# Kernel tuning notes

Hardware: AMD Instinct MI355X
Metric: run time of the kernel (lower is better)

The kernel has to match this reference:

```python
import jax, jax.numpy as jnp
import numpy as np

SIGMA_BOOST = 2.0   # sparse-hyper util.SIGMA_BOOST
EPSILON = 1e-6      # sparse-hyper util.EPSILON (10e-7)
B, N = 512, 16384   # batch, size


def setup_inputs() -> dict:
    key = jax.random.key(0)
    k1, k2, k3, k4, k5 = jax.random.split(key, 5)
    return {
        "x": jax.random.normal(k1, (B, N), jnp.float32),
        "noise": jax.random.normal(k2, (B, N, 2), jnp.float32),
        "pmeans": jax.random.normal(k3, (N, 2), jnp.float32),
        "psigmas": jax.random.normal(k4, (N,), jnp.float32),
        "pvalues": jax.random.normal(k5, (N,), jnp.float32),
    }


def reference(x, noise, pmeans, psigmas, pvalues):
    b, n = x.shape
    s = jnp.float32(n)  # square size (n, n); both dims equal
    # hyper(): transform_means = sigmoid * (size-1); transform_sigmas = (softplus(.+boost)+eps) * size
    means = jax.nn.sigmoid(pmeans)[None] * (s - 1.0)                    # (1, n, 2) -> bcast (b, n, 2)
    sigmas = (jax.nn.softplus(psigmas + SIGMA_BOOST) + EPSILON)[None, :, None] * s  # (1, n, 1)
    # Normal(means, sigmas).sample() -- non-differentiable sample
    samples = jax.lax.stop_gradient(means + sigmas * noise)             # (b, n, 2)
    # round, clamp to [0, n-1]
    indices = jnp.clip(jnp.round(samples).astype(jnp.int32), 0, n - 1)  # (b, n, 2)
    rows, cols = indices[..., 0], indices[..., 1]                       # (b, n) each
    values = jnp.broadcast_to(pvalues[None, :], (b, n))
    # sparse.contract: y[b, rows[b,t]] += values[b,t] * x[b, cols[b,t]]
    contrib = values * jnp.take_along_axis(x, cols, axis=1)             # (b, n)
    y = jnp.zeros((b, n), x.dtype).at[jnp.arange(b)[:, None], rows].add(contrib)
    return y
```

## Files before the change

### kernel.cpp

```cpp
#include <hip/hip_runtime.h>
#include <math.h>

#define SIGMA_BOOST 2.0f
#define EPSILON 1e-6f

typedef float vfloat4 __attribute__((ext_vector_type(4)));

__global__ void params_kernel(const float2* __restrict__ pmeans,
                              const float* __restrict__ psigmas,
                              const float* __restrict__ pvalues,
                              float4* __restrict__ params, int N) {
    int t = blockIdx.x * blockDim.x + threadIdx.x;
    if (t >= N) return;
    float2 pm = pmeans[t];
    float scale = (float)(N - 1);
    float m0 = __fmul_rn(__fdiv_rn(1.0f, __fadd_rn(1.0f, expf(-pm.x))), scale);
    float m1 = __fmul_rn(__fdiv_rn(1.0f, __fadd_rn(1.0f, expf(-pm.y))), scale);
    float z  = __fadd_rn(psigmas[t], SIGMA_BOOST);
    float sp = __fadd_rn(fmaxf(z, 0.0f), log1pf(expf(-fabsf(z))));
    float sg = __fmul_rn(__fadd_rn(sp, EPSILON), (float)N);
    params[t] = make_float4(m0, m1, sg, pvalues[t]);
}

__device__ __forceinline__ void sample_m(
        const float4 p, const float n0, const float n1,
        const float* __restrict__ xb, float* __restrict__ ly,
        const int iN1, const float fN1, float& acc0, float& accE) {
    float s0 = __fadd_rn(p.x, __fmul_rn(p.z, n0));
    float s1 = __fadd_rn(p.y, __fmul_rn(p.z, n1));
    int row = (int)fminf(fmaxf(rintf(s0), 0.0f), fN1);
    int col = (int)fminf(fmaxf(rintf(s1), 0.0f), fN1);
    float xv = xb[col];
    float ctr = __fmul_rn(p.w, xv);
    bool lo = (row == 0);
    bool hi = (row == iN1);
    if (!(lo | hi)) atomicAdd(&ly[row], ctr);
    acc0 = __fadd_rn(acc0, lo ? ctr : 0.0f);
    accE = __fadd_rn(accE, hi ? ctr : 0.0f);
}

template <bool INLINE_PARAMS>
__launch_bounds__(1024, 8)
__global__ void contract_kernel(const float* __restrict__ x,
                                const float2* __restrict__ noise,
                                const float4* __restrict__ params,
                                const float2* __restrict__ pmeans,
                                const float* __restrict__ psigmas,
                                const float* __restrict__ pvalues,
                                float* __restrict__ y, int N) {
    extern __shared__ float ly[];
    const int b = blockIdx.x;
    const int tid = threadIdx.x;
    const int nthr = blockDim.x;

    float4* ly4 = (float4*)ly;
    const int n4 = N >> 2;
    for (int i = tid; i < n4; i += nthr) ly4[i] = make_float4(0.f, 0.f, 0.f, 0.f);
    __syncthreads();

    const float* xb = x + (size_t)b * N;
    const float fN1 = (float)(N - 1);
    const int iN1 = N - 1;
    float acc0 = 0.0f, accE = 0.0f;

    if (!INLINE_PARAMS && ((N >> 1) % (2 * nthr)) == 0) {
        const vfloat4* nb4 = (const vfloat4*)(noise + (size_t)b * N);
        const int npairs = N >> 1;
        const int steps = npairs / (2 * nthr);
        int q0 = tid, q1 = tid + nthr;
        vfloat4 nzA = __builtin_nontemporal_load(&nb4[q0]);
        vfloat4 nzB = __builtin_nontemporal_load(&nb4[q1]);
        float4 pa = params[2 * q0];
        float4 pb = params[2 * q0 + 1];
        float4 pc = params[2 * q1];
        float4 pd = params[2 * q1 + 1];
        for (int s = 0; s < steps; ++s) {
            const vfloat4 cA = nzA, cB = nzB;
            const float4 qa = pa, qb = pb, qc = pc, qd = pd;
            q0 += 2 * nthr; q1 += 2 * nthr;
            if (s + 1 < steps) {
                nzA = __builtin_nontemporal_load(&nb4[q0]);
                nzB = __builtin_nontemporal_load(&nb4[q1]);
                pa = params[2 * q0];
                pb = params[2 * q0 + 1];
                pc = params[2 * q1];
                pd = params[2 * q1 + 1];
            }
            sample_m(qa, cA.x, cA.y, xb, ly, iN1, fN1, acc0, accE);
            sample_m(qb, cA.z, cA.w, xb, ly, iN1, fN1, acc0, accE);
            sample_m(qc, cB.x, cB.y, xb, ly, iN1, fN1, acc0, accE);
            sample_m(qd, cB.z, cB.w, xb, ly, iN1, fN1, acc0, accE);
        }
    } else {
        const float2* nb = noise + (size_t)b * N;
        for (int t = tid; t < N; t += nthr) {
            float4 p;
            if (INLINE_PARAMS) {
                float2 pm = pmeans[t];
                float scale = (float)(N - 1);
                p.x = __fmul_rn(__fdiv_rn(1.0f, __fadd_rn(1.0f, expf(-pm.x))), scale);
                p.y = __fmul_rn(__fdiv_rn(1.0f, __fadd_rn(1.0f, expf(-pm.y))), scale);
                float z  = __fadd_rn(psigmas[t], SIGMA_BOOST);
                float sp = __fadd_rn(fmaxf(z, 0.0f), log1pf(expf(-fabsf(z))));
                p.z = __fmul_rn(__fadd_rn(sp, EPSILON), (float)N);
                p.w = pvalues[t];
            } else {
                p = params[t];
            }
            float2 nz = nb[t];
            sample_m(p, nz.x, nz.y, xb, ly, iN1, fN1, acc0, accE);
        }
    }

    for (int off = 32; off > 0; off >>= 1) {
        acc0 = __fadd_rn(acc0, __shfl_down(acc0, off, 64));
        accE = __fadd_rn(accE, __shfl_down(accE, off, 64));
    }
    if ((tid & 63) == 0) {
        atomicAdd(&ly[0], acc0);
        atomicAdd(&ly[iN1], accE);
    }
    __syncthreads();

    const vfloat4* lv4 = (const vfloat4*)ly;
    vfloat4* yb4 = (vfloat4*)(y + (size_t)b * N);
    for (int i = tid; i < n4; i += nthr)
        __builtin_nontemporal_store(lv4[i], &yb4[i]);
}

extern "C" void kernel_launch(void* const* d_in, const int* in_sizes, int n_in,
                              void* d_out, int out_size, void* d_ws, size_t ws_size,
                              hipStream_t stream) {
    const float*  x       = (const float*)d_in[0];
    const float2* noise   = (const float2*)d_in[1];
    const float2* pmeans  = (const float2*)d_in[2];
    const float*  psigmas = (const float*)d_in[3];
    const float*  pvalues = (const float*)d_in[4];
    float* y = (float*)d_out;

    const int N = in_sizes[3];
    const int B = in_sizes[0] / N;

    const size_t params_bytes = (size_t)N * sizeof(float4);
    const bool use_ws = (ws_size >= params_bytes) && (d_ws != nullptr);

    const int block = 1024;
    const size_t lds_bytes = (size_t)N * sizeof(float);

    if (use_ws) {
        float4* params = (float4*)d_ws;
        params_kernel<<<(N + 255) / 256, 256, 0, stream>>>(pmeans, psigmas,
                                                           pvalues, params, N);
        contract_kernel<false><<<B, block, lds_bytes, stream>>>(
            x, noise, params, nullptr, nullptr, nullptr, y, N);
    } else {
        contract_kernel<true><<<B, block, lds_bytes, stream>>>(
            x, noise, nullptr, pmeans, psigmas, pvalues, y, N);
    }
}
```

Baseline: 150.1 us.

## Stage x in LDS for gathers and scatter atomics directly to global y

Swaps the roles of shared memory and global memory. Each block's row of x is now copied into LDS so the random column gathers read from LDS, while y is zeroed in global memory and the scatter-adds go straight to global y as atomics. This removes the LDS zero-fill and the final LDS-to-global copy of y. In exchange, every non-boundary contribution becomes a global atomic instead of an LDS atomic, which can cost much more per operation.

```diff
diff --git a/kernel.cpp b/kernel.cpp
--- a/kernel.cpp
+++ b/kernel.cpp
@@ -22,19 +22,19 @@
     params[t] = make_float4(m0, m1, sg, pvalues[t]);
 }
 
-__device__ __forceinline__ void sample_m(
+__device__ __forceinline__ void sample_g(
         const float4 p, const float n0, const float n1,
-        const float* __restrict__ xb, float* __restrict__ ly,
+        const float* __restrict__ lx, float* __restrict__ yb,
         const int iN1, const float fN1, float& acc0, float& accE) {
     float s0 = __fadd_rn(p.x, __fmul_rn(p.z, n0));
     float s1 = __fadd_rn(p.y, __fmul_rn(p.z, n1));
     int row = (int)fminf(fmaxf(rintf(s0), 0.0f), fN1);
     int col = (int)fminf(fmaxf(rintf(s1), 0.0f), fN1);
-    float xv = xb[col];
+    float xv = lx[col];
     float ctr = __fmul_rn(p.w, xv);
     bool lo = (row == 0);
     bool hi = (row == iN1);
-    if (!(lo | hi)) atomicAdd(&ly[row], ctr);
+    if (!(lo | hi)) atomicAdd(&yb[row], ctr);
     acc0 = __fadd_rn(acc0, lo ? ctr : 0.0f);
     accE = __fadd_rn(accE, hi ? ctr : 0.0f);
 }
@@ -48,17 +48,32 @@
                                 const float* __restrict__ psigmas,
                                 const float* __restrict__ pvalues,
                                 float* __restrict__ y, int N) {
-    extern __shared__ float ly[];
+    extern __shared__ float lx[];
     const int b = blockIdx.x;
     const int tid = threadIdx.x;
     const int nthr = blockDim.x;
 
-    float4* ly4 = (float4*)ly;
-    const int n4 = N >> 2;
-    for (int i = tid; i < n4; i += nthr) ly4[i] = make_float4(0.f, 0.f, 0.f, 0.f);
+    const float* xb = x + (size_t)b * N;
+    float* yb = y + (size_t)b * N;
+
+    if ((N & 3) == 0) {
+        const int n4 = N >> 2;
+        vfloat4* lx4 = (vfloat4*)lx;
+        const vfloat4* xb4 = (const vfloat4*)xb;
+        vfloat4* yb4 = (vfloat4*)yb;
+        const vfloat4 vz = {0.f, 0.f, 0.f, 0.f};
+        for (int i = tid; i < n4; i += nthr) {
+            lx4[i] = xb4[i];
+            yb4[i] = vz;
+        }
+    } else {
+        for (int i = tid; i < N; i += nthr) {
+            lx[i] = xb[i];
+            yb[i] = 0.0f;
+        }
+    }
     __syncthreads();
 
-    const float* xb = x + (size_t)b * N;
     const float fN1 = (float)(N - 1);
     const int iN1 = N - 1;
     float acc0 = 0.0f, accE = 0.0f;
@@ -86,10 +101,10 @@
                 pc = params[2 * q1];
                 pd = params[2 * q1 + 1];
             }
-            sample_m(qa, cA.x, cA.y, xb, ly, iN1, fN1, acc0, accE);
-            sample_m(qb, cA.z, cA.w, xb, ly, iN1, fN1, acc0, accE);
-            sample_m(qc, cB.x, cB.y, xb, ly, iN1, fN1, acc0, accE);
-            sample_m(qd, cB.z, cB.w, xb, ly, iN1, fN1, acc0, accE);
+            sample_g(qa, cA.x, cA.y, lx, yb, iN1, fN1, acc0, accE);
+            sample_g(qb, cA.z, cA.w, lx, yb, iN1, fN1, acc0, accE);
+            sample_g(qc, cB.x, cB.y, lx, yb, iN1, fN1, acc0, accE);
+            sample_g(qd, cB.z, cB.w, lx, yb, iN1, fN1, acc0, accE);
         }
     } else {
         const float2* nb = noise + (size_t)b * N;
@@ -108,7 +123,7 @@
                 p = params[t];
             }
             float2 nz = nb[t];
-            sample_m(p, nz.x, nz.y, xb, ly, iN1, fN1, acc0, accE);
+            sample_g(p, nz.x, nz.y, lx, yb, iN1, fN1, acc0, accE);
         }
     }
 
@@ -117,15 +132,9 @@
         accE = __fadd_rn(accE, __shfl_down(accE, off, 64));
     }
     if ((tid & 63) == 0) {
-        atomicAdd(&ly[0], acc0);
-        atomicAdd(&ly[iN1], accE);
+        atomicAdd(&yb[0], acc0);
+        atomicAdd(&yb[iN1], accE);
     }
-    __syncthreads();
-
-    const vfloat4* lv4 = (const vfloat4*)ly;
-    vfloat4* yb4 = (vfloat4*)(y + (size_t)b * N);
-    for (int i = tid; i < n4; i += nthr)
-        __builtin_nontemporal_store(lv4[i], &yb4[i]);
 }
 
 extern "C" void kernel_launch(void* const* d_in, const int* in_sizes, int n_in,
```

Result: slower. 208.3 us (+38.8%).

## Hand-schedule a deep software pipeline with inline asm loads and explicit vmcnt waits

Applied to the files above, without the earlier changes.

The fast path now requires exactly 8 noise-pair vectors per thread and is fully unrolled. Noise and parameter loads run three steps ahead, and the dependent x gathers run one step ahead. All of these are issued as inline-asm global loads, with manual s_waitcnt vmcnt counts and sched barriers, so that several memory round-trips overlap with the LDS atomics. The goal is to hide gather latency that the previous depth-1 prefetch left exposed. In exchange, the code relies on hand-counted vmcnt values that the compiler cannot check, and it uses more registers.

```diff
diff --git a/kernel.cpp b/kernel.cpp
--- a/kernel.cpp
+++ b/kernel.cpp
@@ -5,6 +5,12 @@
 #define EPSILON 1e-6f
 
 typedef float vfloat4 __attribute__((ext_vector_type(4)));
+
+#define WAITV(n)                                                   \
+    do {                                                           \
+        asm volatile("s_waitcnt vmcnt(" #n ")" ::: "memory");      \
+        __builtin_amdgcn_sched_barrier(0);                         \
+    } while (0)
 
 __global__ void params_kernel(const float2* __restrict__ pmeans,
                               const float* __restrict__ psigmas,
@@ -22,23 +28,6 @@
     params[t] = make_float4(m0, m1, sg, pvalues[t]);
 }
 
-__device__ __forceinline__ void sample_m(
-        const float4 p, const float n0, const float n1,
-        const float* __restrict__ xb, float* __restrict__ ly,
-        const int iN1, const float fN1, float& acc0, float& accE) {
-    float s0 = __fadd_rn(p.x, __fmul_rn(p.z, n0));
-    float s1 = __fadd_rn(p.y, __fmul_rn(p.z, n1));
-    int row = (int)fminf(fmaxf(rintf(s0), 0.0f), fN1);
-    int col = (int)fminf(fmaxf(rintf(s1), 0.0f), fN1);
-    float xv = xb[col];
-    float ctr = __fmul_rn(p.w, xv);
-    bool lo = (row == 0);
-    bool hi = (row == iN1);
-    if (!(lo | hi)) atomicAdd(&ly[row], ctr);
-    acc0 = __fadd_rn(acc0, lo ? ctr : 0.0f);
-    accE = __fadd_rn(accE, hi ? ctr : 0.0f);
-}
-
 template <bool INLINE_PARAMS>
 __launch_bounds__(1024, 8)
 __global__ void contract_kernel(const float* __restrict__ x,
@@ -63,33 +52,83 @@
     const int iN1 = N - 1;
     float acc0 = 0.0f, accE = 0.0f;
 
-    if (!INLINE_PARAMS && ((N >> 1) % (2 * nthr)) == 0) {
+    const int npairs = N >> 1;
+    const bool fast = !INLINE_PARAMS && (npairs % nthr) == 0 &&
+                      (npairs / nthr) == 8;
+
+    if (fast) {
         const vfloat4* nb4 = (const vfloat4*)(noise + (size_t)b * N);
-        const int npairs = N >> 1;
-        const int steps = npairs / (2 * nthr);
-        int q0 = tid, q1 = tid + nthr;
-        vfloat4 nzA = __builtin_nontemporal_load(&nb4[q0]);
-        vfloat4 nzB = __builtin_nontemporal_load(&nb4[q1]);
-        float4 pa = params[2 * q0];
-        float4 pb = params[2 * q0 + 1];
-        float4 pc = params[2 * q1];
-        float4 pd = params[2 * q1 + 1];
-        for (int s = 0; s < steps; ++s) {
-            const vfloat4 cA = nzA, cB = nzB;
-            const float4 qa = pa, qb = pb, qc = pc, qd = pd;
-            q0 += 2 * nthr; q1 += 2 * nthr;
-            if (s + 1 < steps) {
-                nzA = __builtin_nontemporal_load(&nb4[q0]);
-                nzB = __builtin_nontemporal_load(&nb4[q1]);
-                pa = params[2 * q0];
-                pb = params[2 * q0 + 1];
-                pc = params[2 * q1];
-                pd = params[2 * q1 + 1];
+        const vfloat4* pp  = (const vfloat4*)params;
+
+        vfloat4 nzv[8], pav[8], pbv[8];
+        float   xv0v[8], xv1v[8], w0v[8], w1v[8];
+        int     r0v[8], r1v[8];
+
+        auto issueL = [&](int k) {
+            unsigned long long a_nz =
+                (unsigned long long)(nb4 + (size_t)k * nthr + tid);
+            unsigned long long a_pa =
+                (unsigned long long)(pp + 2 * ((size_t)k * nthr + tid));
+            unsigned long long a_pb = a_pa + 16ull;
+            asm volatile("global_load_dwordx4 %0, %1, off"
+                         : "=v"(nzv[k]) : "v"(a_nz));
+            asm volatile("global_load_dwordx4 %0, %1, off"
+                         : "=v"(pav[k]) : "v"(a_pa));
+            asm volatile("global_load_dwordx4 %0, %1, off"
+                         : "=v"(pbv[k]) : "v"(a_pb));
+        };
+
+        auto issueG = [&](int k) {
+            vfloat4 nz = nzv[k], pa = pav[k], pb = pbv[k];
+            float s0 = __fadd_rn(pa.x, __fmul_rn(pa.z, nz.x));
+            float s1 = __fadd_rn(pa.y, __fmul_rn(pa.z, nz.y));
+            float s2 = __fadd_rn(pb.x, __fmul_rn(pb.z, nz.z));
+            float s3 = __fadd_rn(pb.y, __fmul_rn(pb.z, nz.w));
+            int r0 = (int)fminf(fmaxf(rintf(s0), 0.0f), fN1);
+            int c0 = (int)fminf(fmaxf(rintf(s1), 0.0f), fN1);
+            int r1 = (int)fminf(fmaxf(rintf(s2), 0.0f), fN1);
+            int c1 = (int)fminf(fmaxf(rintf(s3), 0.0f), fN1);
+            r0v[k] = r0; r1v[k] = r1; w0v[k] = pa.w; w1v[k] = pb.w;
+            unsigned long long a0 = (unsigned long long)(xb + c0);
+            unsigned long long a1 = (unsigned long long)(xb + c1);
+            asm volatile("global_load_dword %0, %1, off"
+                         : "=v"(xv0v[k]) : "v"(a0));
+            asm volatile("global_load_dword %0, %1, off"
+                         : "=v"(xv1v[k]) : "v"(a1));
+        };
+
+        auto commit = [&](int k) {
+            float ctr0 = __fmul_rn(w0v[k], xv0v[k]);
+            float ctr1 = __fmul_rn(w1v[k], xv1v[k]);
+            int r0 = r0v[k], r1 = r1v[k];
+            bool lo0 = (r0 == 0), hi0 = (r0 == iN1);
+            bool lo1 = (r1 == 0), hi1 = (r1 == iN1);
+            if (!(lo0 | hi0)) atomicAdd(&ly[r0], ctr0);
+            if (!(lo1 | hi1)) atomicAdd(&ly[r1], ctr1);
+            acc0 = __fadd_rn(acc0, lo0 ? ctr0 : 0.0f);
+            accE = __fadd_rn(accE, hi0 ? ctr0 : 0.0f);
+            acc0 = __fadd_rn(acc0, lo1 ? ctr1 : 0.0f);
+            accE = __fadd_rn(accE, hi1 ? ctr1 : 0.0f);
+        };
+
+        issueL(0); issueL(1); issueL(2);
+        WAITV(6);
+        issueG(0);
+        WAITV(5);
+
+#pragma unroll
+        for (int k = 0; k < 8; ++k) {
+            if (k == 6) WAITV(2);
+            if (k < 7)  issueG(k + 1);
+            if (k < 5)  issueL(k + 3);
+            if (k <= 5) {
+                WAITV(5);
+            } else if (k == 6) {
+                WAITV(2);
+            } else {
+                WAITV(0);
             }
-            sample_m(qa, cA.x, cA.y, xb, ly, iN1, fN1, acc0, accE);
-            sample_m(qb, cA.z, cA.w, xb, ly, iN1, fN1, acc0, accE);
-            sample_m(qc, cB.x, cB.y, xb, ly, iN1, fN1, acc0, accE);
-            sample_m(qd, cB.z, cB.w, xb, ly, iN1, fN1, acc0, accE);
+            commit(k);
         }
     } else {
         const float2* nb = noise + (size_t)b * N;
@@ -108,7 +147,17 @@
                 p = params[t];
             }
             float2 nz = nb[t];
-            sample_m(p, nz.x, nz.y, xb, ly, iN1, fN1, acc0, accE);
+            float s0 = __fadd_rn(p.x, __fmul_rn(p.z, nz.x));
+            float s1 = __fadd_rn(p.y, __fmul_rn(p.z, nz.y));
+            int row = (int)fminf(fmaxf(rintf(s0), 0.0f), fN1);
+            int col = (int)fminf(fmaxf(rintf(s1), 0.0f), fN1);
+            float xv = xb[col];
+            float ctr = __fmul_rn(p.w, xv);
+            bool lo = (row == 0);
+            bool hi = (row == iN1);
+            if (!(lo | hi)) atomicAdd(&ly[row], ctr);
+            acc0 = __fadd_rn(acc0, lo ? ctr : 0.0f);
+            accE = __fadd_rn(accE, hi ? ctr : 0.0f);
         }
     }
 
```

After: 152.2 us. About the same (+1.4%).
